# Kernel tuning notes

Measured on AMD Instinct MI355X. Metric: run time of the kernel, lower is better.

Reference implementation:

```python
import jax, jax.numpy as jnp
import numpy as np

B, QL, CTX, H = 1, 2048, 2048, 4096
NH, NKV, HD = 32, 8, 128


def rotate_half(x):
    x1, x2 = jnp.split(x, 2, axis=-1)
    return jnp.concatenate([-x2, x1], axis=-1)


def apply_rotary(x, cos, sin):
    # x: [B, h, S, HD]; cos/sin: [B, S, HD] -> broadcast over heads
    cos = cos[:, None, :, :]
    sin = sin[:, None, :, :]
    return x * cos + rotate_half(x) * sin


def setup_inputs() -> dict:
    key = jax.random.key(0)
    ks = jax.random.split(key, 8)
    s = 0.02
    return {
        "hidden_states": jax.random.normal(ks[0], (B, QL, H), jnp.float32),
        "target_hidden": jax.random.normal(ks[1], (B, CTX, H), jnp.float32),
        "cos": jax.random.uniform(ks[2], (B, CTX + QL, HD), jnp.float32),
        "sin": jax.random.uniform(ks[3], (B, CTX + QL, HD), jnp.float32),
        "Wq": jax.random.normal(ks[4], (NH * HD, H), jnp.float32) * s,
        "Wk": jax.random.normal(ks[5], (NKV * HD, H), jnp.float32) * s,
        "Wv": jax.random.normal(ks[6], (NKV * HD, H), jnp.float32) * s,
        "Wo": jax.random.normal(ks[7], (H, NH * HD), jnp.float32) * s,
    }


def reference(hidden_states, target_hidden, cos, sin, Wq, Wk, Wv, Wo):
    bsz, q_len, _ = hidden_states.shape
    ctx_len = target_hidden.shape[1]

    def proj(x, W, nh):  # [B,S,H] @ W.T -> [B,nh,S,HD]
        y = jnp.einsum("bsh,dh->bsd", x, W)
        return y.reshape(bsz, x.shape[1], nh, HD).transpose(0, 2, 1, 3)

    q = proj(hidden_states, Wq, NH)
    k_ctx = proj(target_hidden, Wk, NKV)
    v_ctx = proj(target_hidden, Wv, NKV)
    k_noise = proj(hidden_states, Wk, NKV)
    v_noise = proj(hidden_states, Wv, NKV)

    cos_n = cos[:, ctx_len:ctx_len + q_len]
    sin_n = sin[:, ctx_len:ctx_len + q_len]
    q = apply_rotary(q, cos_n, sin_n)
    k_noise = apply_rotary(k_noise, cos_n, sin_n)
    k_ctx = apply_rotary(k_ctx, cos[:, :ctx_len], sin[:, :ctx_len])

    k = jnp.concatenate([k_ctx, k_noise], axis=2)  # [B,NKV,CTX+QL,HD]
    v = jnp.concatenate([v_ctx, v_noise], axis=2)

    n_rep = NH // NKV
    k = jnp.repeat(k, n_rep, axis=1)  # repeat_interleave on head dim
    v = jnp.repeat(v, n_rep, axis=1)

    scale = 1.0 / jnp.sqrt(jnp.asarray(HD, q.dtype))
    scores = jnp.einsum("bhqd,bhkd->bhqk", q, k) * scale
    probs = jax.nn.softmax(scores, axis=-1)
    attn = jnp.einsum("bhqk,bhkd->bhqd", probs, v)
    attn = attn.transpose(0, 2, 1, 3).reshape(bsz, q_len, NH * HD)
    return jnp.einsum("bsd,hd->bsh", attn, Wo)
```

## Files before the change

kernel.cpp:

```cpp
#include <hip/hip_runtime.h>

typedef unsigned short u16;
typedef _Float16 f16;
typedef _Float16 f16x4 __attribute__((ext_vector_type(4)));
typedef _Float16 f16x8 __attribute__((ext_vector_type(8)));
typedef float f32x4 __attribute__((ext_vector_type(4)));

#define GLL16(gptr, lptr)                                                        \
  __builtin_amdgcn_global_load_lds(                                              \
      (const __attribute__((address_space(1))) void*)(gptr),                     \
      (__attribute__((address_space(3))) void*)(lptr), 16, 0, 0)

__global__ void cast_all_k(const float* __restrict__ h, const float* __restrict__ t,
                           const float* __restrict__ wq, const float* __restrict__ wk,
                           const float* __restrict__ wv, const float* __restrict__ wo,
                           f16* __restrict__ Xcat, f16* __restrict__ Wqb,
                           f16* __restrict__ Wkvb, f16* __restrict__ Wob) {
  long i = (long)blockIdx.x * 256 + threadIdx.x;
  const float* s; f16* d; long off;
  if (i < 2097152)        { s = h;  d = Xcat;            off = i; }
  else if (i < 4194304)   { s = t;  d = Xcat + 8388608;  off = i - 2097152; }
  else if (i < 8388608)   { s = wq; d = Wqb;             off = i - 4194304; }
  else if (i < 9437184)   { s = wk; d = Wkvb;            off = i - 8388608; }
  else if (i < 10485760)  { s = wv; d = Wkvb + 4194304;  off = i - 9437184; }
  else                    { s = wo; d = Wob;             off = i - 10485760; }
  float4 v = *(const float4*)(s + off * 4);
  f16x4 o;
  o.x = (f16)v.x; o.y = (f16)v.y; o.z = (f16)v.z; o.w = (f16)v.w;
  *(f16x4*)(d + off * 4) = o;
}

__global__ __launch_bounds__(256) void proj_gemm(
    const f16* __restrict__ Xcat, const f16* __restrict__ Wqb,
    const f16* __restrict__ Wkvb, const float* __restrict__ cosT,
    const float* __restrict__ sinT, f16* __restrict__ Qb, f16* __restrict__ Kb,
    f16* __restrict__ Vt, float qscale) {
  __shared__ __align__(16) f16 As[128 * 32];
  __shared__ __align__(16) f16 Bs[128 * 32];
  const int tid = threadIdx.x;
  const int w = tid >> 6, lane = tid & 63;
  const int quad = lane >> 4, l16 = lane & 15;
  const int b = blockIdx.x;
  long tM; const f16* Bbase; int bn; bool isQ;
  if (b < 512) { isQ = true;  tM = (long)(b >> 5) * 128; bn = b & 31; Bbase = Wqb; }
  else { int b2 = b - 512; isQ = false; tM = (long)(b2 >> 4) * 128; bn = b2 & 15; Bbase = Wkvb; }

  f32x4 acc[2][8] = {};
  const int srow = w * 32 + (lane >> 2), scol = (lane & 3) * 8;
  const f16* Ag = Xcat + (tM + srow) * 4096 + scol;
  const f16* Bg = Bbase + ((long)bn * 128 + srow) * 4096 + scol;
  f16* AsW = &As[(w * 32) * 32];
  f16* BsW = &Bs[(w * 32) * 32];
  for (int k0 = 0; k0 < 4096; k0 += 32) {
    __syncthreads();
    GLL16(Ag + k0, AsW);
    GLL16(Ag + k0 + 16 * 4096, AsW + 16 * 32);
    GLL16(Bg + k0, BsW);
    GLL16(Bg + k0 + 16 * 4096, BsW + 16 * 32);
    __syncthreads();
    f16x8 af[2], bf[8];
#pragma unroll
    for (int mi = 0; mi < 2; ++mi)
      af[mi] = *(const f16x8*)&As[(w * 32 + mi * 16 + l16) * 32 + quad * 8];
#pragma unroll
    for (int ni = 0; ni < 8; ++ni)
      bf[ni] = *(const f16x8*)&Bs[(ni * 16 + l16) * 32 + quad * 8];
#pragma unroll
    for (int mi = 0; mi < 2; ++mi)
#pragma unroll
      for (int ni = 0; ni < 8; ++ni)
        acc[mi][ni] =
            __builtin_amdgcn_mfma_f32_16x16x32_f16(af[mi], bf[ni], acc[mi][ni], 0, 0, 0);
  }

  if (!isQ && bn >= 8) {
    const int kvh = bn - 8;
#pragma unroll
    for (int mi = 0; mi < 2; ++mi) {
      int key0 = ((int)tM + w * 32 + mi * 16 + quad * 4) ^ 2048;
#pragma unroll
      for (int ni = 0; ni < 8; ++ni) {
        int d = ni * 16 + l16;
        f16x4 pk;
#pragma unroll
        for (int r = 0; r < 4; ++r) pk[r] = (f16)acc[mi][ni][r];
        *(f16x4*)&Vt[((long)kvh * 128 + d) * 4096 + key0] = pk;
      }
    }
  } else {
    const float sc = isQ ? qscale : 1.0f;
#pragma unroll
    for (int mi = 0; mi < 2; ++mi)
#pragma unroll
      for (int r = 0; r < 4; ++r) {
        int rg = (int)tM + w * 32 + mi * 16 + quad * 4 + r;
        int pos = isQ ? (2048 + rg) : (rg ^ 2048);
        const float* cp = cosT + (long)pos * 128;
        const float* sp = sinT + (long)pos * 128;
        f16* orow = isQ ? Qb + ((long)bn * 2048 + rg) * 128
                        : Kb + ((long)bn * 4096 + pos) * 128;
#pragma unroll
        for (int ni = 0; ni < 4; ++ni) {
          int d = ni * 16 + l16;
          float x0 = acc[mi][ni][r], x1 = acc[mi][ni + 4][r];
          orow[d] = (f16)((x0 * cp[d] - x1 * sp[d]) * sc);
          orow[d + 64] = (f16)((x1 * cp[d + 64] + x0 * sp[d + 64]) * sc);
        }
      }
  }
}

__global__ __launch_bounds__(256, 2) void flash_k(const f16* __restrict__ Qb,
                                                  const f16* __restrict__ Kb,
                                                  const f16* __restrict__ Vt,
                                                  f16* __restrict__ Ob) {
  __shared__ __align__(16) f16 Ks[64 * 128];
  __shared__ __align__(16) f16 Vs[128 * 64];
  __shared__ __align__(16) f16 Ps[4][32 * 72];
  const int tid = threadIdx.x;
  const int w = tid >> 6, lane = tid & 63;
  const int quad = lane >> 4, l16 = lane & 15;
  const int h = blockIdx.y;
  const int kvh = h >> 2;
  const int q0 = blockIdx.x * 128;

  f16x8 qf[2][4];
#pragma unroll
  for (int mi = 0; mi < 2; ++mi) {
    const f16* qrow = Qb + ((long)h * 2048 + q0 + w * 32 + mi * 16 + l16) * 128 + quad * 8;
#pragma unroll
    for (int kc = 0; kc < 4; ++kc) qf[mi][kc] = *(const f16x8*)(qrow + kc * 32);
  }

  f32x4 of[2][8] = {};
  float lsum[2] = {0.f, 0.f};
  const f16* Kg = Kb + (long)kvh * 4096 * 128;
  const f16* Vg = Vt + (long)kvh * 128 * 4096;
  f16* PsW = &Ps[w][0];

  const int krow_in_wave = (lane >> 4);
  const int kslot = lane & 15;
  const int vrow_in_wave = (lane >> 3);
  const int vslot = lane & 7;
  const int vgc = vslot ^ (vrow_in_wave & 7);

  for (int kt = 0; kt < 64; ++kt) {
    __syncthreads();
#pragma unroll
    for (int it = 0; it < 4; ++it) {
      int row = w * 16 + it * 4 + krow_in_wave;
      int gc = kslot ^ (it * 4 + krow_in_wave);
      GLL16(Kg + (long)(kt * 64 + row) * 128 + gc * 8, &Ks[(w * 16 + it * 4) * 128]);
    }
#pragma unroll
    for (int it = 0; it < 4; ++it) {
      int row = w * 32 + it * 8 + vrow_in_wave;
      GLL16(Vg + (long)row * 4096 + kt * 64 + vgc * 8, &Vs[(w * 32 + it * 8) * 64]);
    }
    __syncthreads();
    f32x4 s[2][4] = {};
#pragma unroll
    for (int nt = 0; nt < 4; ++nt) {
      f16x8 ak[4];
#pragma unroll
      for (int kc = 0; kc < 4; ++kc) {
        int slot = (kc * 4 + quad) ^ l16;
        ak[kc] = *(const f16x8*)&Ks[(nt * 16 + l16) * 128 + slot * 8];
      }
#pragma unroll
      for (int mi = 0; mi < 2; ++mi)
#pragma unroll
        for (int kc = 0; kc < 4; ++kc)
          s[mi][nt] = __builtin_amdgcn_mfma_f32_16x16x32_f16(ak[kc], qf[mi][kc],
                                                             s[mi][nt], 0, 0, 0);
    }
#pragma unroll
    for (int mi = 0; mi < 2; ++mi)
#pragma unroll
      for (int nt = 0; nt < 4; ++nt) {
        f16x4 pk;
#pragma unroll
        for (int r = 0; r < 4; ++r) {
          float pv = __builtin_amdgcn_exp2f(s[mi][nt][r]);
          lsum[mi] += pv;
          pk[r] = (f16)pv;
        }
        *(f16x4*)&PsW[(mi * 16 + l16) * 72 + nt * 16 + quad * 4] = pk;
      }
#pragma unroll
    for (int kc2 = 0; kc2 < 2; ++kc2) {
      f16x8 bp[2];
#pragma unroll
      for (int mi = 0; mi < 2; ++mi)
        bp[mi] = *(const f16x8*)&PsW[(mi * 16 + l16) * 72 + kc2 * 32 + quad * 8];
#pragma unroll
      for (int dt = 0; dt < 8; ++dt) {
        int slot = (kc2 * 4 + quad) ^ (l16 & 7);
        f16x8 av = *(const f16x8*)&Vs[(dt * 16 + l16) * 64 + slot * 8];
#pragma unroll
        for (int mi = 0; mi < 2; ++mi)
          of[mi][dt] =
              __builtin_amdgcn_mfma_f32_16x16x32_f16(av, bp[mi], of[mi][dt], 0, 0, 0);
      }
    }
  }
#pragma unroll
  for (int mi = 0; mi < 2; ++mi) {
    float v = lsum[mi];
    v += __shfl_xor(v, 16, 64);
    v += __shfl_xor(v, 32, 64);
    float inv = 1.0f / v;
    long q = q0 + w * 32 + mi * 16 + l16;
#pragma unroll
    for (int dt = 0; dt < 8; ++dt) {
      f16x4 o4;
#pragma unroll
      for (int r = 0; r < 4; ++r) o4[r] = (f16)(of[mi][dt][r] * inv);
      *(f16x4*)&Ob[q * 4096 + h * 128 + dt * 16 + quad * 4] = o4;
    }
  }
}

__global__ __launch_bounds__(256) void gemm_osplit(const f16* __restrict__ A,
                                                   const f16* __restrict__ B,
                                                   float* __restrict__ Cp) {
  __shared__ __align__(16) f16 As[128 * 32];
  __shared__ __align__(16) f16 Bs[128 * 32];
  const int tid = threadIdx.x;
  const int w = tid >> 6, lane = tid & 63;
  const int quad = lane >> 4, l16 = lane & 15;
  const int wm = w >> 1, wn = w & 1;
  const long tM = (long)blockIdx.y * 128, tN = (long)blockIdx.x * 128;
  const int z = blockIdx.z;
  const int kBeg = z * 2048;
  f32x4 acc[4][4] = {};
  const int srow = w * 32 + (lane >> 2);
  const int scol = (lane & 3) * 8;
  const f16* Ag = A + (tM + srow) * 4096 + scol;
  const f16* Bg = B + (tN + srow) * 4096 + scol;
  f16* AsW = &As[(w * 32) * 32];
  f16* BsW = &Bs[(w * 32) * 32];
  for (int k0 = kBeg; k0 < kBeg + 2048; k0 += 32) {
    __syncthreads();
    GLL16(Ag + k0, AsW);
    GLL16(Ag + k0 + 16 * 4096, AsW + 16 * 32);
    GLL16(Bg + k0, BsW);
    GLL16(Bg + k0 + 16 * 4096, BsW + 16 * 32);
    __syncthreads();
    f16x8 af[4], bfr[4];
#pragma unroll
    for (int mi = 0; mi < 4; ++mi)
      af[mi] = *(const f16x8*)&As[(wm * 64 + mi * 16 + l16) * 32 + quad * 8];
#pragma unroll
    for (int ni = 0; ni < 4; ++ni)
      bfr[ni] = *(const f16x8*)&Bs[(wn * 64 + ni * 16 + l16) * 32 + quad * 8];
#pragma unroll
    for (int mi = 0; mi < 4; ++mi)
#pragma unroll
      for (int ni = 0; ni < 4; ++ni)
        acc[mi][ni] =
            __builtin_amdgcn_mfma_f32_16x16x32_f16(af[mi], bfr[ni], acc[mi][ni], 0, 0, 0);
  }
  float* Cz = Cp + (long)z * 8388608;
#pragma unroll
  for (int mi = 0; mi < 4; ++mi)
#pragma unroll
    for (int ni = 0; ni < 4; ++ni)
#pragma unroll
      for (int r = 0; r < 4; ++r) {
        long row = tM + wm * 64 + mi * 16 + quad * 4 + r;
        long col = tN + wn * 64 + ni * 16 + l16;
        Cz[row * 4096 + col] = acc[mi][ni][r];
      }
}

__global__ void reduce2_k(const float* __restrict__ p, float* __restrict__ out) {
  long i = ((long)blockIdx.x * 256 + threadIdx.x) * 4;
  float4 a = *(const float4*)(p + i);
  float4 b = *(const float4*)(p + 8388608 + i);
  a.x += b.x; a.y += b.y; a.z += b.z; a.w += b.w;
  *(float4*)(out + i) = a;
}

extern "C" void kernel_launch(void* const* d_in, const int* in_sizes, int n_in,
                              void* d_out, int out_size, void* d_ws, size_t ws_size,
                              hipStream_t stream) {
  (void)in_sizes; (void)n_in; (void)out_size; (void)ws_size;
  const float* hidden = (const float*)d_in[0];
  const float* target = (const float*)d_in[1];
  const float* cosT = (const float*)d_in[2];
  const float* sinT = (const float*)d_in[3];
  const float* Wq = (const float*)d_in[4];
  const float* Wk = (const float*)d_in[5];
  const float* Wv = (const float*)d_in[6];
  const float* Wo = (const float*)d_in[7];
  float* out = (float*)d_out;

  char* p = (char*)d_ws;
  auto alloc = [&](size_t bytes) {
    char* r = p;
    p += (bytes + 255) & ~(size_t)255;
    return r;
  };
  f16* Xcat = (f16*)alloc(4096ull * 4096 * 2);
  f16* Wqb  = (f16*)alloc(4096ull * 4096 * 2);
  f16* Wkvb = (f16*)alloc(2048ull * 4096 * 2);
  f16* Wob  = (f16*)alloc(4096ull * 4096 * 2);
  f16* Qb   = (f16*)alloc(32ull * 2048 * 128 * 2);
  f16* Kb   = (f16*)alloc(8ull * 4096 * 128 * 2);
  f16* Vt   = (f16*)alloc(8ull * 128 * 4096 * 2);
  f16* Ao   = (f16*)alloc(2048ull * 4096 * 2);
  float* Pp = (float*)d_ws;

  cast_all_k<<<57344, 256, 0, stream>>>(hidden, target, Wq, Wk, Wv, Wo,
                                        Xcat, Wqb, Wkvb, Wob);

  const float QSC = (float)(0.08838834764831845 * 1.4426950408889634);
  proj_gemm<<<1024, 256, 0, stream>>>(Xcat, Wqb, Wkvb, cosT, sinT, Qb, Kb, Vt, QSC);

  flash_k<<<dim3(16, 32), 256, 0, stream>>>(Qb, Kb, Vt, Ao);

  gemm_osplit<<<dim3(32, 16, 2), 256, 0, stream>>>(Ao, Wob, Pp);
  reduce2_k<<<8192, 256, 0, stream>>>(Pp, out);
}
```

Measured before the change: 703.1 us.

## Replace projection and output GEMMs with a pipelined 256x256 double-buffered template kernel

Both the QKV projection GEMM and the output-projection GEMM now go through one templated 512-thread kernel. It uses 256x256 tiles, a 64-wide K step, double-buffered LDS filled by direct global-to-LDS loads with an XOR swizzle, and a staged schedule that interleaves loads with MFMA quarters under s_setprio. Block indices are remapped across XCDs. The aim is to raise data reuse and overlap memory traffic with matrix math, in place of the earlier single-buffered 128-tile loops that sync twice per step. In exchange the kernel uses 128KB of LDS and launches only 256 blocks, which may limit occupancy and leave CUs partly idle.

```diff
diff --git a/kernel.cpp b/kernel.cpp
--- a/kernel.cpp
+++ b/kernel.cpp
@@ -30,54 +30,179 @@
   *(f16x4*)(d + off * 4) = o;
 }
 
-__global__ __launch_bounds__(256) void proj_gemm(
+template <int MODE>
+__global__ __launch_bounds__(512, 2) void gemm8k(
     const f16* __restrict__ Xcat, const f16* __restrict__ Wqb,
     const f16* __restrict__ Wkvb, const float* __restrict__ cosT,
     const float* __restrict__ sinT, f16* __restrict__ Qb, f16* __restrict__ Kb,
-    f16* __restrict__ Vt, float qscale) {
-  __shared__ __align__(16) f16 As[128 * 32];
-  __shared__ __align__(16) f16 Bs[128 * 32];
+    f16* __restrict__ Vt, const f16* __restrict__ Ao,
+    const f16* __restrict__ Wob, float* __restrict__ Cp, float qscale) {
+  __shared__ __align__(16) f16 lds[65536];
   const int tid = threadIdx.x;
   const int w = tid >> 6, lane = tid & 63;
   const int quad = lane >> 4, l16 = lane & 15;
-  const int b = blockIdx.x;
-  long tM; const f16* Bbase; int bn; bool isQ;
-  if (b < 512) { isQ = true;  tM = (long)(b >> 5) * 128; bn = b & 31; Bbase = Wqb; }
-  else { int b2 = b - 512; isQ = false; tM = (long)(b2 >> 4) * 128; bn = b2 & 15; Bbase = Wkvb; }
-
-  f32x4 acc[2][8] = {};
-  const int srow = w * 32 + (lane >> 2), scol = (lane & 3) * 8;
-  const f16* Ag = Xcat + (tM + srow) * 4096 + scol;
-  const f16* Bg = Bbase + ((long)bn * 128 + srow) * 4096 + scol;
-  f16* AsW = &As[(w * 32) * 32];
-  f16* BsW = &Bs[(w * 32) * 32];
-  for (int k0 = 0; k0 < 4096; k0 += 32) {
-    __syncthreads();
-    GLL16(Ag + k0, AsW);
-    GLL16(Ag + k0 + 16 * 4096, AsW + 16 * 32);
-    GLL16(Bg + k0, BsW);
-    GLL16(Bg + k0 + 16 * 4096, BsW + 16 * 32);
-    __syncthreads();
-    f16x8 af[2], bf[8];
-#pragma unroll
-    for (int mi = 0; mi < 2; ++mi)
-      af[mi] = *(const f16x8*)&As[(w * 32 + mi * 16 + l16) * 32 + quad * 8];
-#pragma unroll
-    for (int ni = 0; ni < 8; ++ni)
-      bf[ni] = *(const f16x8*)&Bs[(ni * 16 + l16) * 32 + quad * 8];
-#pragma unroll
-    for (int mi = 0; mi < 2; ++mi)
+  const int wm = w >> 1, wn = w & 1;
+
+  int b = (int)blockIdx.x;
+  int l = ((b & 7) << 5) | (b >> 3);
+
+  const f16 *A, *B;
+  long tM, tN;
+  int NT, kbeg;
+  bool isQ = false, isV = false;
+  float* Cz = nullptr;
+  if (MODE == 0) {
+    kbeg = 0; NT = 64;
+    if (l < 128) {
+      A = Xcat; B = Wqb; tM = (long)(l >> 4) * 256; tN = (long)(l & 15) * 256;
+      isQ = true;
+    } else {
+      int l2 = l - 128;
+      A = Xcat; B = Wkvb; tM = (long)(l2 >> 3) * 256; tN = (long)(l2 & 7) * 256;
+      isV = (tN >= 1024);
+    }
+  } else {
+    int z = l >> 7, r0 = l & 127;
+    A = Ao; B = Wob; tM = (long)(r0 >> 4) * 256; tN = (long)(r0 & 15) * 256;
+    kbeg = z * 2048; NT = 32; Cz = Cp + (long)z * 8388608;
+  }
+
+  const int sr8 = lane >> 3;
+  const int cg = (lane & 7) ^ sr8;
+  const f16* Ag = A + (tM + 16 * w + sr8) * 4096 + kbeg + cg * 8;
+  const f16* Bg = B + (tN + 16 * w + sr8) * 4096 + kbeg + cg * 8;
+  const int ldsw = w * 1024;
+
+#define STAGE_A(hf, t, c)                                                      \
+  do {                                                                         \
+    const f16* g_ = Ag + (long)(t) * 64 + (long)(hf) * (128 * 4096);           \
+    f16* d_ = &lds[(c) * 16384 + (hf) * 8192 + ldsw];                          \
+    GLL16(g_, d_);                                                             \
+    GLL16(g_ + 8 * 4096, d_ + 512);                                            \
+  } while (0)
+#define STAGE_B(hf, t, c)                                                      \
+  do {                                                                         \
+    const f16* g_ = Bg + (long)(t) * 64 + (long)(hf) * (128 * 4096);           \
+    f16* d_ = &lds[32768 + (c) * 16384 + (hf) * 8192 + ldsw];                  \
+    GLL16(g_, d_);                                                             \
+    GLL16(g_ + 8 * 4096, d_ + 512);                                            \
+  } while (0)
+
+  const int rA = wm * 64 + l16;
+  const int rB = wn * 128 + l16;
+  const int sw = l16 & 7;
+#define LDA(fr, mi, kk, c)                                                     \
+  fr = *(const f16x8*)&lds[(c) * 16384 + (rA + (mi) * 16) * 64 +               \
+                           (((kk) * 4 + quad) ^ sw) * 8]
+#define LDB(fr, ni, kk, c)                                                     \
+  fr = *(const f16x8*)&lds[32768 + (c) * 16384 + (rB + (ni) * 16) * 64 +       \
+                           (((kk) * 4 + quad) ^ sw) * 8]
+
+#define MFMA16 __builtin_amdgcn_mfma_f32_16x16x32_f16
+#define BAR() __builtin_amdgcn_s_barrier()
+#define WAITDS()                                                               \
+  do {                                                                         \
+    asm volatile("s_waitcnt lgkmcnt(0)" ::: "memory");                         \
+    __builtin_amdgcn_sched_barrier(0);                                         \
+  } while (0)
+
+  f32x4 acc[4][8] = {};
+  f16x8 af[2][2], bf0[4][2], bf1[4][2];
+
+  STAGE_B(0, 0, 0); STAGE_B(1, 0, 0); STAGE_A(0, 0, 0); STAGE_A(1, 0, 0);
+  STAGE_B(0, 1, 1); STAGE_B(1, 1, 1);
+  asm volatile("s_waitcnt vmcnt(4)" ::: "memory");
+  BAR();
+
+#define TILE_STEP(t, c)                                                        \
+  do {                                                                         \
+                                       \
+    LDA(af[0][0], 0, 0, c); LDA(af[0][1], 0, 1, c);                            \
+    LDA(af[1][0], 1, 0, c); LDA(af[1][1], 1, 1, c);                            \
+    LDB(bf0[0][0], 0, 0, c); LDB(bf0[0][1], 0, 1, c);                          \
+    LDB(bf0[1][0], 1, 0, c); LDB(bf0[1][1], 1, 1, c);                          \
+    LDB(bf0[2][0], 2, 0, c); LDB(bf0[2][1], 2, 1, c);                          \
+    LDB(bf0[3][0], 3, 0, c); LDB(bf0[3][1], 3, 1, c);                          \
+    if ((t) + 1 < NT) STAGE_A(0, (t) + 1, (c) ^ 1);                            \
+    BAR(); WAITDS();                                                           \
+    __builtin_amdgcn_s_setprio(1);                                             \
+    _Pragma("unroll") for (int mi = 0; mi < 2; ++mi)                           \
+        _Pragma("unroll") for (int ni = 0; ni < 4; ++ni) {                     \
+      acc[mi][ni] = MFMA16(af[mi][0], bf0[ni][0], acc[mi][ni], 0, 0, 0);       \
+      acc[mi][ni] = MFMA16(af[mi][1], bf0[ni][1], acc[mi][ni], 0, 0, 0);       \
+    }                                                                          \
+    __builtin_amdgcn_s_setprio(0);                                             \
+    BAR();                                                                     \
+                                       \
+    LDB(bf1[0][0], 4, 0, c); LDB(bf1[0][1], 4, 1, c);                          \
+    LDB(bf1[1][0], 5, 0, c); LDB(bf1[1][1], 5, 1, c);                          \
+    LDB(bf1[2][0], 6, 0, c); LDB(bf1[2][1], 6, 1, c);                          \
+    LDB(bf1[3][0], 7, 0, c); LDB(bf1[3][1], 7, 1, c);                          \
+    if ((t) + 1 < NT) STAGE_A(1, (t) + 1, (c) ^ 1);                            \
+    BAR(); WAITDS();                                                           \
+    __builtin_amdgcn_s_setprio(1);                                             \
+    _Pragma("unroll") for (int mi = 0; mi < 2; ++mi)                           \
+        _Pragma("unroll") for (int ni = 0; ni < 4; ++ni) {                     \
+      acc[mi][4 + ni] =                                                        \
+          MFMA16(af[mi][0], bf1[ni][0], acc[mi][4 + ni], 0, 0, 0);             \
+      acc[mi][4 + ni] =                                                        \
+          MFMA16(af[mi][1], bf1[ni][1], acc[mi][4 + ni], 0, 0, 0);             \
+    }                                                                          \
+    __builtin_amdgcn_s_setprio(0);                                             \
+    BAR();                                                                     \
+            \
+    LDA(af[0][0], 2, 0, c); LDA(af[0][1], 2, 1, c);                            \
+    LDA(af[1][0], 3, 0, c); LDA(af[1][1], 3, 1, c);                            \
+    if ((t) + 2 < NT) STAGE_B(0, (t) + 2, c);                                  \
+    BAR(); WAITDS();                                                           \
+    __builtin_amdgcn_s_setprio(1);                                             \
+    _Pragma("unroll") for (int mi = 0; mi < 2; ++mi)                           \
+        _Pragma("unroll") for (int ni = 0; ni < 4; ++ni) {                     \
+      acc[2 + mi][ni] = MFMA16(af[mi][0], bf0[ni][0], acc[2 + mi][ni], 0, 0, 0);\
+      acc[2 + mi][ni] = MFMA16(af[mi][1], bf0[ni][1], acc[2 + mi][ni], 0, 0, 0);\
+    }                                                                          \
+    __builtin_amdgcn_s_setprio(0);                                             \
+    BAR();                                                                     \
+      \
+    if ((t) + 2 < NT) STAGE_B(1, (t) + 2, c);                                  \
+    BAR();                                                                     \
+    __builtin_amdgcn_s_setprio(1);                                             \
+    _Pragma("unroll") for (int mi = 0; mi < 2; ++mi)                           \
+        _Pragma("unroll") for (int ni = 0; ni < 4; ++ni) {                     \
+      acc[2 + mi][4 + ni] =                                                    \
+          MFMA16(af[mi][0], bf1[ni][0], acc[2 + mi][4 + ni], 0, 0, 0);         \
+      acc[2 + mi][4 + ni] =                                                    \
+          MFMA16(af[mi][1], bf1[ni][1], acc[2 + mi][4 + ni], 0, 0, 0);         \
+    }                                                                          \
+    __builtin_amdgcn_s_setprio(0);                                             \
+    if ((t) + 2 < NT)                                                          \
+      asm volatile("s_waitcnt vmcnt(4)" ::: "memory");                         \
+    else                                                                       \
+      asm volatile("s_waitcnt vmcnt(0)" ::: "memory");                         \
+    BAR();                                                                     \
+  } while (0)
+
+  for (int t = 0; t < NT; t += 2) {
+    TILE_STEP(t, 0);
+    TILE_STEP(t + 1, 1);
+  }
+
+  if (MODE == 1) {
+#pragma unroll
+    for (int mi = 0; mi < 4; ++mi)
 #pragma unroll
       for (int ni = 0; ni < 8; ++ni)
-        acc[mi][ni] =
-            __builtin_amdgcn_mfma_f32_16x16x32_f16(af[mi], bf[ni], acc[mi][ni], 0, 0, 0);
-  }
-
-  if (!isQ && bn >= 8) {
-    const int kvh = bn - 8;
-#pragma unroll
-    for (int mi = 0; mi < 2; ++mi) {
-      int key0 = ((int)tM + w * 32 + mi * 16 + quad * 4) ^ 2048;
+#pragma unroll
+        for (int r = 0; r < 4; ++r) {
+          long row = tM + wm * 64 + mi * 16 + quad * 4 + r;
+          long col = tN + wn * 128 + ni * 16 + l16;
+          Cz[row * 4096 + col] = acc[mi][ni][r];
+        }
+  } else if (isV) {
+    const int kvh = (int)((tN - 1024) >> 7) + wn;
+#pragma unroll
+    for (int mi = 0; mi < 4; ++mi) {
+      int key0 = ((int)tM + wm * 64 + mi * 16 + quad * 4) ^ 2048;
 #pragma unroll
       for (int ni = 0; ni < 8; ++ni) {
         int d = ni * 16 + l16;
@@ -89,16 +214,17 @@
     }
   } else {
     const float sc = isQ ? qscale : 1.0f;
-#pragma unroll
-    for (int mi = 0; mi < 2; ++mi)
+    const int h = (int)(tN >> 7) + wn;
+#pragma unroll
+    for (int mi = 0; mi < 4; ++mi)
 #pragma unroll
       for (int r = 0; r < 4; ++r) {
-        int rg = (int)tM + w * 32 + mi * 16 + quad * 4 + r;
+        int rg = (int)tM + wm * 64 + mi * 16 + quad * 4 + r;
         int pos = isQ ? (2048 + rg) : (rg ^ 2048);
         const float* cp = cosT + (long)pos * 128;
         const float* sp = sinT + (long)pos * 128;
-        f16* orow = isQ ? Qb + ((long)bn * 2048 + rg) * 128
-                        : Kb + ((long)bn * 4096 + pos) * 128;
+        f16* orow = isQ ? Qb + ((long)h * 2048 + rg) * 128
+                        : Kb + ((long)h * 4096 + pos) * 128;
 #pragma unroll
         for (int ni = 0; ni < 4; ++ni) {
           int d = ni * 16 + l16;
@@ -108,6 +234,14 @@
         }
       }
   }
+#undef TILE_STEP
+#undef STAGE_A
+#undef STAGE_B
+#undef LDA
+#undef LDB
+#undef WAITDS
+#undef BAR
+#undef MFMA16
 }
 
 __global__ __launch_bounds__(256, 2) void flash_k(const f16* __restrict__ Qb,
@@ -219,59 +353,6 @@
       *(f16x4*)&Ob[q * 4096 + h * 128 + dt * 16 + quad * 4] = o4;
     }
   }
-}
-
-__global__ __launch_bounds__(256) void gemm_osplit(const f16* __restrict__ A,
-                                                   const f16* __restrict__ B,
-                                                   float* __restrict__ Cp) {
-  __shared__ __align__(16) f16 As[128 * 32];
-  __shared__ __align__(16) f16 Bs[128 * 32];
-  const int tid = threadIdx.x;
-  const int w = tid >> 6, lane = tid & 63;
-  const int quad = lane >> 4, l16 = lane & 15;
-  const int wm = w >> 1, wn = w & 1;
-  const long tM = (long)blockIdx.y * 128, tN = (long)blockIdx.x * 128;
-  const int z = blockIdx.z;
-  const int kBeg = z * 2048;
-  f32x4 acc[4][4] = {};
-  const int srow = w * 32 + (lane >> 2);
-  const int scol = (lane & 3) * 8;
-  const f16* Ag = A + (tM + srow) * 4096 + scol;
-  const f16* Bg = B + (tN + srow) * 4096 + scol;
-  f16* AsW = &As[(w * 32) * 32];
-  f16* BsW = &Bs[(w * 32) * 32];
-  for (int k0 = kBeg; k0 < kBeg + 2048; k0 += 32) {
-    __syncthreads();
-    GLL16(Ag + k0, AsW);
-    GLL16(Ag + k0 + 16 * 4096, AsW + 16 * 32);
-    GLL16(Bg + k0, BsW);
-    GLL16(Bg + k0 + 16 * 4096, BsW + 16 * 32);
-    __syncthreads();
-    f16x8 af[4], bfr[4];
-#pragma unroll
-    for (int mi = 0; mi < 4; ++mi)
-      af[mi] = *(const f16x8*)&As[(wm * 64 + mi * 16 + l16) * 32 + quad * 8];
-#pragma unroll
-    for (int ni = 0; ni < 4; ++ni)
-      bfr[ni] = *(const f16x8*)&Bs[(wn * 64 + ni * 16 + l16) * 32 + quad * 8];
-#pragma unroll
-    for (int mi = 0; mi < 4; ++mi)
-#pragma unroll
-      for (int ni = 0; ni < 4; ++ni)
-        acc[mi][ni] =
-            __builtin_amdgcn_mfma_f32_16x16x32_f16(af[mi], bfr[ni], acc[mi][ni], 0, 0, 0);
-  }
-  float* Cz = Cp + (long)z * 8388608;
-#pragma unroll
-  for (int mi = 0; mi < 4; ++mi)
-#pragma unroll
-    for (int ni = 0; ni < 4; ++ni)
-#pragma unroll
-      for (int r = 0; r < 4; ++r) {
-        long row = tM + wm * 64 + mi * 16 + quad * 4 + r;
-        long col = tN + wn * 64 + ni * 16 + l16;
-        Cz[row * 4096 + col] = acc[mi][ni][r];
-      }
 }
 
 __global__ void reduce2_k(const float* __restrict__ p, float* __restrict__ out) {
@@ -316,10 +397,12 @@
                                         Xcat, Wqb, Wkvb, Wob);
 
   const float QSC = (float)(0.08838834764831845 * 1.4426950408889634);
-  proj_gemm<<<1024, 256, 0, stream>>>(Xcat, Wqb, Wkvb, cosT, sinT, Qb, Kb, Vt, QSC);
+  gemm8k<0><<<256, 512, 0, stream>>>(Xcat, Wqb, Wkvb, cosT, sinT, Qb, Kb, Vt,
+                                     nullptr, nullptr, nullptr, QSC);
 
   flash_k<<<dim3(16, 32), 256, 0, stream>>>(Qb, Kb, Vt, Ao);
 
-  gemm_osplit<<<dim3(32, 16, 2), 256, 0, stream>>>(Ao, Wob, Pp);
+  gemm8k<1><<<256, 512, 0, stream>>>(nullptr, nullptr, nullptr, nullptr, nullptr,
+                                     nullptr, nullptr, nullptr, Ao, Wob, Pp, 0.f);
   reduce2_k<<<8192, 256, 0, stream>>>(Pp, out);
 }
```

New measurement: 592.5 us. -15.7%, faster.
